# Performance work log

Measured on AMD Instinct MI355X. Metric: run time of the kernel, lower is better.

Reference implementation:

```python
import jax, jax.numpy as jnp
import numpy as np

DT = 0.001
TAU_SYN_INV = 200.0  # norse default 1/5e-3
TAU_MEM_INV = 100.0  # norse default 1/1e-2
V_TH = 0.4
ALPHA = 10.0  # SuperSpike surrogate slope


@jax.custom_vjp
def heaviside(x):
    # SuperSpike: heaviside forward, 1/(alpha*|x|+1)^2 surrogate backward
    return (x > 0).astype(x.dtype)

def _h_fwd(x):
    return heaviside(x), x

def _h_bwd(x, g):
    return (g / (ALPHA * jnp.abs(x) + 1.0) ** 2,)

heaviside.defvjp(_h_fwd, _h_bwd)


def conv(x, w, b, stride=1):
    y = jax.lax.conv_general_dilated(
        x, w, (stride, stride), 'VALID',
        dimension_numbers=('NCHW', 'OIHW', 'NCHW'))
    return y + b[None, :, None, None]


def maxpool2(x):
    return jax.lax.reduce_window(x, -jnp.inf, jax.lax.max, (1, 1, 2, 2), (1, 1, 2, 2), 'VALID')


def setup_inputs() -> dict:
    key = jax.random.key(0)
    ks = jax.random.split(key, 11)
    B, T, H, W = 32, 64, 64, 64
    num_classes = 10
    F = 96 * 12 * 12  # flattened encoder size = 13824
    HID = 128

    def u(k, shape, fan_in):
        bound = 1.0 / np.sqrt(fan_in)
        return jax.random.uniform(k, shape, jnp.float32, -bound, bound)

    return dict(
        x=jax.random.normal(ks[0], (B, T, 1, H, W), jnp.float32),
        w1=u(ks[1], (32, 1, 5, 5), 25), b1=u(ks[2], (32,), 25),
        w2=u(ks[3], (64, 32, 3, 3), 32 * 9), b2=u(ks[4], (64,), 32 * 9),
        w3=u(ks[5], (96, 64, 3, 3), 64 * 9), b3=u(ks[6], (96,), 64 * 9),
        w_in=jax.random.normal(ks[7], (HID, F), jnp.float32) / np.sqrt(F),
        w_rec=jax.random.normal(ks[8], (HID, HID), jnp.float32) / np.sqrt(HID),
        w_fc=u(ks[9], (num_classes, HID), HID),
        b_fc=u(ks[10], (num_classes,), HID),
    )


def reference(x, w1, b1, w2, b2, w3, b3, w_in, w_rec, w_fc, b_fc):
    B, T = x.shape[0], x.shape[1]
    HID = w_in.shape[0]
    C = w_fc.shape[0]

    # encoder vectorized over all B*T frames
    frames = x.reshape(B * T, x.shape[2], x.shape[3], x.shape[4])
    z = jax.nn.relu(conv(frames, w1, b1, stride=2))  # [BT,32,30,30]
    z = jax.nn.relu(conv(z, w2, b2))                 # [BT,64,28,28]
    z = maxpool2(z)                                  # [BT,64,14,14]
    z = jax.nn.relu(conv(z, w3, b3))                 # [BT,96,12,12]
    feats = z.reshape(B, T, -1)                      # [B,T,13824]

    # precompute feed-forward input currents for all timesteps
    ff = jnp.einsum('btf,hf->tbh', feats, w_in)      # [T,B,HID]

    def step(carry, ff_t):
        z_p, v, i, vr, ir = carry
        # LIF recurrent cell (norse lif_step, v_leak=0, v_reset=0)
        v_dec = v + DT * TAU_MEM_INV * (-v + i)
        i_dec = i - DT * TAU_SYN_INV * i
        z_n = heaviside(v_dec - V_TH)
        v_n = (1.0 - z_n) * v_dec
        i_n = i_dec + ff_t + z_p @ w_rec.T  # recurrent uses previous spikes
        # readout linear + LI cell (norse li_feed_forward_step)
        ro = z_n @ w_fc.T + b_fc
        vr_n = vr + DT * TAU_MEM_INV * (-vr + ir)
        ir_n = ir - DT * TAU_SYN_INV * ir + ro
        return (z_n, v_n, i_n, vr_n, ir_n), vr_n

    zeros_h = jnp.zeros((B, HID), x.dtype)
    zeros_c = jnp.zeros((B, C), x.dtype)
    carry0 = (zeros_h, zeros_h, zeros_h, zeros_c, zeros_c)
    _, voltages = jax.lax.scan(step, carry0, ff)     # [T,B,C]

    out = jnp.max(voltages, axis=0)                  # [B,C]
    return jax.nn.log_softmax(out, axis=1)
```

## Files before the change

### kernel.cpp

```cpp
#include <hip/hip_runtime.h>
#include <math.h>

typedef _Float16 half8 __attribute__((ext_vector_type(8)));
typedef _Float16 half4 __attribute__((ext_vector_type(4)));
typedef float f32x16 __attribute__((ext_vector_type(16)));

__global__ __launch_bounds__(256) void xprep_k(const float* __restrict__ x,
                                               _Float16* __restrict__ xh,
                                               _Float16* __restrict__ xl) {
  const int i = blockIdx.x * 256 + threadIdx.x;
  if (i >= 2097152) return;
  const float4 v = *(const float4*)(x + (size_t)i * 4);
  half4 h, l;
  const float vv[4] = {v.x, v.y, v.z, v.w};
#pragma unroll
  for (int e = 0; e < 4; ++e) {
    const _Float16 hh = (_Float16)vv[e];
    h[e] = hh;
    l[e] = (_Float16)((vv[e] - (float)hh) * 1024.0f);
  }
  *(half4*)(xh + (size_t)i * 4) = h;
  *(half4*)(xl + (size_t)i * 4) = l;
}

__global__ __launch_bounds__(256) void w1prep_k(const float* __restrict__ w1,
                                                _Float16* __restrict__ w1p) {
  const int i = blockIdx.x * 256 + threadIdx.x;
  if (i >= 1024) return;
  const int blk = i >> 8;
  const int s = blk >> 1, g = blk & 1;
  const int ch = (i >> 3) & 31, e = i & 7;
  const int k = s * 16 + g * 8 + e;
  float v = 0.f;
  if (k < 25) v = w1[ch * 25 + k];
  const _Float16 h = (_Float16)v;
  w1p[i] = h;
  w1p[1024 + i] = (_Float16)((v - (float)h) * 1024.0f);
}

__global__ __launch_bounds__(256) void w2prep_k(const float* __restrict__ w2,
                                                _Float16* __restrict__ w2p) {
  const int i = blockIdx.x * 256 + threadIdx.x;
  if (i >= 18432) return;
  const int tap = i >> 11;
  const int r = i & 2047;
  const int blk = r >> 8;
  const int nt = blk >> 2, s = (blk >> 1) & 1, g = blk & 1;
  const int n = (r >> 3) & 31, e = r & 7;
  const int och = nt * 32 + n;
  const int ic = s * 16 + g * 8 + e;
  const float v = w2[och * 288 + ic * 9 + tap];
  const _Float16 h = (_Float16)v;
  const _Float16 l = (_Float16)((v - (float)h) * 1024.0f);
  w2p[i] = h;
  w2p[18432 + i] = l;
}

__global__ __launch_bounds__(256) void w3prep_k(const float* __restrict__ w3,
                                                _Float16* __restrict__ w3p) {
  const int i = blockIdx.x * 256 + threadIdx.x;
  if (i >= 55296) return;
  const int icc = i / 27648;
  const int r1 = i - icc * 27648;
  const int tc = r1 / 6144;
  const int rem = r1 - tc * 6144;
  const int tl = rem / 3072;
  const int rem2 = rem - tl * 3072;
  const int nt = rem2 >> 10;
  const int s = (rem2 >> 9) & 1;
  const int g = (rem2 >> 8) & 1;
  const int n = (rem2 >> 3) & 31;
  const int e = rem2 & 7;
  const int tap = tc * 2 + tl;
  const int och = nt * 32 + n;
  const int ic = icc * 32 + s * 16 + g * 8 + e;
  const float v = w3[(size_t)och * 576 + ic * 9 + tap];
  const _Float16 h = (_Float16)v;
  const _Float16 l = (_Float16)((v - (float)h) * 1024.0f);
  w3p[i] = h;
  w3p[55296 + i] = l;
}

__global__ __launch_bounds__(256) void winprep_k(const float* __restrict__ w_in,
                                                 _Float16* __restrict__ winp) {
  const int i = blockIdx.x * 256 + threadIdx.x;
  if (i >= 1769472) return;
  const int ks = i >> 11;
  const int rem = i & 2047;
  const int nt = rem >> 9;
  const int g = (rem >> 8) & 1;
  const int n = (rem >> 3) & 31;
  const int e = rem & 7;
  const int h = nt * 32 + n;
  const int k = ks * 16 + g * 8 + e;
  const float v = w_in[(size_t)h * 13824 + k];
  const _Float16 hh = (_Float16)v;
  const _Float16 ll = (_Float16)((v - (float)hh) * 1024.0f);
  winp[i] = hh;
  winp[1769472 + i] = ll;
}

__global__ __launch_bounds__(448) void conv2f_mfma_k(
    const _Float16* __restrict__ xh, const _Float16* __restrict__ xl,
    const float* __restrict__ b1, const _Float16* __restrict__ w1p,
    const _Float16* __restrict__ w2p, const float* __restrict__ b2,
    _Float16* __restrict__ y2s) {
  __shared__ __align__(16) _Float16 S[24960];
  const int rp = blockIdx.x;
  const int img0 = blockIdx.y * 2;
  const int tid = threadIdx.x;

  const int w = tid >> 6;
  const int lane = tid & 63;
  const int l31 = lane & 31;
  const int g = lane >> 5;

  {
    const float b1c = b1[l31];
    const int gb = l31 >> 3, e0 = l31 & 7;
    int xoffs[16];
#pragma unroll
    for (int s = 0; s < 2; ++s)
#pragma unroll
      for (int e = 0; e < 8; ++e) {
        const int k = s * 16 + g * 8 + e;
        const int ky = k / 5, kx = k - (k / 5) * 5;
        xoffs[s * 8 + e] = (k < 25) ? (ky * 64 + kx) : -1;
      }
#pragma unroll 1
    for (int ph = 0; ph < 2; ++ph) {
      if (tid < 240) {
        const int plane = tid / 120;
        const int c8 = tid - plane * 120;
        const _Float16* src = (plane ? xl : xh) +
                              (size_t)(img0 + ph) * 4096 + rp * 512 + c8 * 8;
        *(float4*)&S[23040 + plane * 960 + c8 * 8] = *(const float4*)src;
      }
      __syncthreads();
      if (w < 6) {
        const int p = w * 32 + l31;
        const int pcl = (p < 180) ? p : 179;
        const int row = pcl / 30;
        const int col = pcl - row * 30;
        const int xb = (2 * row) * 64 + 2 * col;
        f32x16 acc_h = {}, acc_l = {};
#pragma unroll
        for (int s = 0; s < 2; ++s) {
          half8 ah, al;
#pragma unroll
          for (int e = 0; e < 8; ++e) {
            const int o = xoffs[s * 8 + e];
            _Float16 hv = (_Float16)0.f, lv = (_Float16)0.f;
            if (o >= 0) {
              hv = S[23040 + xb + o];
              lv = S[24000 + xb + o];
            }
            ah[e] = hv;
            al[e] = lv;
          }
          const _Float16* bp = w1p + ((s * 2 + g) * 32 + l31) * 8;
          half8 bh = *(const half8*)bp;
          half8 bl = *(const half8*)(bp + 1024);
          acc_h = __builtin_amdgcn_mfma_f32_32x32x16_f16(ah, bh, acc_h, 0, 0, 0);
          acc_l = __builtin_amdgcn_mfma_f32_32x32x16_f16(ah, bl, acc_l, 0, 0, 0);
          acc_l = __builtin_amdgcn_mfma_f32_32x32x16_f16(al, bh, acc_l, 0, 0, 0);
        }
#pragma unroll
        for (int r = 0; r < 16; ++r) {
          const int mrow = (r & 3) + 8 * (r >> 2) + 4 * g;
          const int pp = w * 32 + mrow;
          if (pp < 180) {
            const int cl = pp - (pp / 30) * 30;
            const int swz = (cl >> 1) & 3;
            const int addr = ph * 5760 + pp * 32 + ((gb ^ swz) << 3) + e0;
            const float val =
                fmaxf(acc_h[r] + acc_l[r] * 9.765625e-4f + b1c, 0.f);
            const _Float16 hh = (_Float16)val;
            S[addr] = hh;
            S[11520 + addr] = (_Float16)((val - (float)hh) * 1024.0f);
          }
        }
      }
      __syncthreads();
    }
  }

  const int m = w * 32 + l31;
  const int aimg = m / 112;
  const int apos = m - aimg * 112;
  const int ar = apos / 28;
  const int ax = apos - ar * 28;
  const int icg = g * 8;

  f32x16 acc00 = {}, acc01 = {}, acc10 = {}, acc11 = {};

  const _Float16* bb = w2p + g * 256 + l31 * 8;
  half8 pbh0, pbl0, pbh1, pbl1;
  half8 qbh0, qbl0, qbh1, qbl1;
  {
    pbh0 = *(const half8*)&bb[0];
    pbl0 = *(const half8*)&bb[18432];
    pbh1 = *(const half8*)&bb[1024];
    pbl1 = *(const half8*)&bb[18432 + 1024];
  }
#pragma unroll 1
  for (int i = 0; i < 18; i += 2) {
    {
      const int tap = (i + 1) >> 1, s = (i + 1) & 1;
      const _Float16* bt = bb + tap * 2048 + s * 512;
      qbh0 = *(const half8*)&bt[0];
      qbl0 = *(const half8*)&bt[18432];
      qbh1 = *(const half8*)&bt[1024];
      qbl1 = *(const half8*)&bt[18432 + 1024];
    }
    {
      const int tap = i >> 1, s = i & 1;
      const int ky = tap / 3, kx = tap - (tap / 3) * 3;
      const int acol = ax + kx;
      const int swzA = ((acol >> 1) & 3) << 3;
      const int abase = aimg * 5760 + ((ar + ky) * 30 + acol) * 32;
      const int icoA = (s * 16 + icg) ^ swzA;
      half8 ah = *(const half8*)&S[abase + icoA];
      half8 al = *(const half8*)&S[11520 + abase + icoA];
      acc00 = __builtin_amdgcn_mfma_f32_32x32x16_f16(ah, pbh0, acc00, 0, 0, 0);
      acc10 = __builtin_amdgcn_mfma_f32_32x32x16_f16(ah, pbl0, acc10, 0, 0, 0);
      acc10 = __builtin_amdgcn_mfma_f32_32x32x16_f16(al, pbh0, acc10, 0, 0, 0);
      acc01 = __builtin_amdgcn_mfma_f32_32x32x16_f16(ah, pbh1, acc01, 0, 0, 0);
      acc11 = __builtin_amdgcn_mfma_f32_32x32x16_f16(ah, pbl1, acc11, 0, 0, 0);
      acc11 = __builtin_amdgcn_mfma_f32_32x32x16_f16(al, pbh1, acc11, 0, 0, 0);
    }
    if (i + 2 < 18) {
      const int tap = (i + 2) >> 1, s = (i + 2) & 1;
      const _Float16* bt = bb + tap * 2048 + s * 512;
      pbh0 = *(const half8*)&bt[0];
      pbl0 = *(const half8*)&bt[18432];
      pbh1 = *(const half8*)&bt[1024];
      pbl1 = *(const half8*)&bt[18432 + 1024];
    }
    {
      const int ii = i + 1;
      const int tap = ii >> 1, s = ii & 1;
      const int ky = tap / 3, kx = tap - (tap / 3) * 3;
      const int acol = ax + kx;
      const int swzA = ((acol >> 1) & 3) << 3;
      const int abase = aimg * 5760 + ((ar + ky) * 30 + acol) * 32;
      const int icoA = (s * 16 + icg) ^ swzA;
      half8 ah = *(const half8*)&S[abase + icoA];
      half8 al = *(const half8*)&S[11520 + abase + icoA];
      acc00 = __builtin_amdgcn_mfma_f32_32x32x16_f16(ah, qbh0, acc00, 0, 0, 0);
      acc10 = __builtin_amdgcn_mfma_f32_32x32x16_f16(ah, qbl0, acc10, 0, 0, 0);
      acc10 = __builtin_amdgcn_mfma_f32_32x32x16_f16(al, qbh0, acc10, 0, 0, 0);
      acc01 = __builtin_amdgcn_mfma_f32_32x32x16_f16(ah, qbh1, acc01, 0, 0, 0);
      acc11 = __builtin_amdgcn_mfma_f32_32x32x16_f16(ah, qbl1, acc11, 0, 0, 0);
      acc11 = __builtin_amdgcn_mfma_f32_32x32x16_f16(al, qbh1, acc11, 0, 0, 0);
    }
  }

  float* sPool = (float*)S;
#pragma unroll 1
  for (int ph = 0; ph < 2; ++ph) {
    __syncthreads();
#pragma unroll
    for (int r = 0; r < 16; ++r) {
      const int mrow = (r & 3) + 8 * (r >> 2) + 4 * g;
      const int mo = w * 32 + mrow;
      const int srow = mo - ph * 112;
      if (srow >= 0 && srow < 112) {
        sPool[srow * 68 + l31] = acc00[r] + acc10[r] * 9.765625e-4f;
        sPool[srow * 68 + 32 + l31] = acc01[r] + acc11[r] * 9.765625e-4f;
      }
    }
    __syncthreads();
    if (tid < 224) {
      const int pr = tid / 112;
      const int r2 = tid - pr * 112;
      const int pc = r2 >> 3;
      const int blk = r2 & 7;
      const int m00 = pr * 56 + pc * 2;
      const float* s0 = &sPool[m00 * 68 + blk * 8];
      float rowv[4][8];
      *(float4*)&rowv[0][0] = *(const float4*)s0;
      *(float4*)&rowv[0][4] = *(const float4*)(s0 + 4);
      *(float4*)&rowv[1][0] = *(const float4*)(s0 + 68);
      *(float4*)&rowv[1][4] = *(const float4*)(s0 + 72);
      *(float4*)&rowv[2][0] = *(const float4*)(s0 + 28 * 68);
      *(float4*)&rowv[2][4] = *(const float4*)(s0 + 28 * 68 + 4);
      *(float4*)&rowv[3][0] = *(const float4*)(s0 + 29 * 68);
      *(float4*)&rowv[3][4] = *(const float4*)(s0 + 29 * 68 + 4);
      half8 hv, lv;
#pragma unroll
      for (int e = 0; e < 8; ++e) {
        const float mx = fmaxf(fmaxf(rowv[0][e], rowv[1][e]),
                               fmaxf(rowv[2][e], rowv[3][e]));
        const float val = fmaxf(mx + b2[blk * 8 + e], 0.f);
        const _Float16 hh = (_Float16)val;
        hv[e] = hh;
        lv[e] = (_Float16)((val - (float)hh) * 1024.0f);
      }
      const int posg = (rp * 2 + pr) * 14 + pc;
      const int icc = blk >> 2;
      const int slot = (blk & 3) ^ ((posg >> 1) & 3);
      _Float16* dh = y2s + (size_t)(img0 + ph) * 25088 + icc * 6272 +
                     posg * 32 + slot * 8;
      *(float4*)dh = *(float4*)&hv;
      *(float4*)(dh + 12544) = *(float4*)&lv;
    }
  }
}

__global__ __launch_bounds__(320) void conv3_mfma_k(
    const _Float16* __restrict__ y2s, const _Float16* __restrict__ w3p,
    const float* __restrict__ b3, _Float16* __restrict__ fh,
    _Float16* __restrict__ fl) {
  __shared__ __align__(16) _Float16 S[12544];
  const int img = blockIdx.x;
  const int tid = threadIdx.x;
  const int w = tid >> 6;
  const int lane = tid & 63;
  const int l31 = lane & 31;
  const int g = lane >> 5;
  const int m = w * 32 + l31;
  const int mc = (m < 144) ? m : 143;
  const int r = mc / 12, c = mc - (mc / 12) * 12;

  f32x16 acch[3] = {};
  f32x16 accl[3] = {};

  const _Float16* bb = w3p + g * 256 + l31 * 8;
#pragma unroll 1
  for (int icc = 0; icc < 2; ++icc) {
    __syncthreads();
    {
      const _Float16* src = y2s + (size_t)img * 25088 + icc * 6272;
      for (int c8 = tid; c8 < 784; c8 += 320) {
        *(float4*)&S[c8 * 8] = *(const float4*)&src[c8 * 8];
        *(float4*)&S[6272 + c8 * 8] = *(const float4*)&src[12544 + c8 * 8];
      }
    }
    __syncthreads();
#pragma unroll 1
    for (int tc = 0; tc < 5; ++tc) {
      const int ntaps = (tc == 4) ? 1 : 2;
#pragma unroll 1
      for (int tl = 0; tl < ntaps; ++tl) {
        const int tap = tc * 2 + tl;
        const int ky = tap / 3, kx = tap - (tap / 3) * 3;
        const int pix = (r + ky) * 14 + (c + kx);
        const int pswz = (pix >> 1) & 3;
        half8 ah[2], al[2];
#pragma unroll
        for (int s = 0; s < 2; ++s) {
          const int o = pix * 32 + ((s * 2 + g) ^ pswz) * 8;
          ah[s] = *(const half8*)&S[o];
          al[s] = *(const half8*)&S[6272 + o];
        }
        const _Float16* bt = bb + icc * 27648 + tc * 6144 + tl * 3072;
#pragma unroll
        for (int nt = 0; nt < 3; ++nt) {
#pragma unroll
          for (int s = 0; s < 2; ++s) {
            const _Float16* bp = bt + nt * 1024 + s * 512;
            half8 bh = *(const half8*)bp;
            half8 bl = *(const half8*)(bp + 55296);
            acch[nt] =
                __builtin_amdgcn_mfma_f32_32x32x16_f16(ah[s], bh, acch[nt], 0, 0, 0);
            accl[nt] =
                __builtin_amdgcn_mfma_f32_32x32x16_f16(ah[s], bl, accl[nt], 0, 0, 0);
            accl[nt] =
                __builtin_amdgcn_mfma_f32_32x32x16_f16(al[s], bh, accl[nt], 0, 0, 0);
          }
        }
      }
    }
  }
  float* sO = (float*)S;
#pragma unroll
  for (int nt = 0; nt < 3; ++nt) {
    __syncthreads();
#pragma unroll
    for (int rr = 0; rr < 16; ++rr) {
      const int row = (rr & 3) + 8 * (rr >> 2) + 4 * g;
      const int pos = w * 32 + row;
      if (pos < 144)
        sO[l31 * 145 + pos] = acch[nt][rr] + accl[nt][rr] * 9.765625e-4f;
    }
    __syncthreads();
    for (int idx8 = tid; idx8 < 576; idx8 += 320) {
      const int oc = idx8 / 18;
      const int pb = idx8 - oc * 18;
      const float bb2 = b3[nt * 32 + oc];
      half8 hv, lv;
#pragma unroll
      for (int e = 0; e < 8; ++e) {
        const float v = fmaxf(sO[oc * 145 + pb * 8 + e] + bb2, 0.f);
        const _Float16 hh = (_Float16)v;
        hv[e] = hh;
        lv[e] = (_Float16)((v - (float)hh) * 1024.0f);
      }
      const size_t ko = (size_t)img * 13824 + (nt * 32 + oc) * 144 + pb * 8;
      *(float4*)&fh[ko] = *(float4*)&hv;
      *(float4*)&fl[ko] = *(float4*)&lv;
    }
  }
}

__global__ __launch_bounds__(256) void ffgemm_k(
    const _Float16* __restrict__ fh, const _Float16* __restrict__ fl,
    const _Float16* __restrict__ winp, float* __restrict__ P, int frame0,
    int Cl) {
  __shared__ __align__(16) _Float16 S[24576];
  const int mb = blockIdx.x;
  const int kc = blockIdx.y;
  const int tid = threadIdx.x;
  const int w = tid >> 6;
  const int lane = tid & 63;
  const int l31 = lane & 31;
  const int g = lane >> 5;
  const int mt = w >> 1;
  const int nt0 = (w & 1) * 2;
  f32x16 acc_h[2] = {};
  f32x16 acc_l[2] = {};
  const int kbase = kc * 1728;
#pragma unroll 1
  for (int kt = 0; kt < 27; ++kt) {
    __syncthreads();
    for (int i = tid; i < 512; i += 256) {
      const int row = i >> 3, kb = i & 7;
      int rc = mb * 64 + row;
      if (rc >= Cl) rc = Cl - 1;
      const size_t so = (size_t)rc * 13824 + kbase + kt * 64 + kb * 8;
      const int d = row * 64 + ((kb ^ (row & 7)) * 8);
      *(float4*)&S[d] = *(const float4*)&fh[so];
      *(float4*)&S[4096 + d] = *(const float4*)&fl[so];
    }
    {
      const size_t bo = (size_t)(kc * 108 + kt * 4) * 2048;
      for (int i = tid; i < 1024; i += 256) {
        *(float4*)&S[8192 + i * 8] = *(const float4*)&winp[bo + i * 8];
        *(float4*)&S[16384 + i * 8] =
            *(const float4*)&winp[1769472 + bo + i * 8];
      }
    }
    __syncthreads();
#pragma unroll
    for (int ks = 0; ks < 4; ++ks) {
      const int kb = ks * 2 + g;
      const int ao = (mt * 32 + l31) * 64 + ((kb ^ (l31 & 7)) * 8);
      half8 ah = *(const half8*)&S[ao];
      half8 al = *(const half8*)&S[4096 + ao];
#pragma unroll
      for (int j = 0; j < 2; ++j) {
        const int nt = nt0 + j;
        const int b = 8192 + (((ks * 4 + nt) * 2 + g) * 32 + l31) * 8;
        half8 bh = *(const half8*)&S[b];
        half8 bl = *(const half8*)&S[8192 + b];
        acc_h[j] = __builtin_amdgcn_mfma_f32_32x32x16_f16(ah, bh, acc_h[j], 0, 0, 0);
        acc_l[j] = __builtin_amdgcn_mfma_f32_32x32x16_f16(ah, bl, acc_l[j], 0, 0, 0);
        acc_l[j] = __builtin_amdgcn_mfma_f32_32x32x16_f16(al, bh, acc_l[j], 0, 0, 0);
      }
    }
  }
  float* Pp = P + ((size_t)kc * 2048 + (size_t)frame0) * 128;
#pragma unroll
  for (int j = 0; j < 2; ++j) {
    const int h = (nt0 + j) * 32 + l31;
#pragma unroll
    for (int r = 0; r < 16; ++r) {
      const int row = (r & 3) + 8 * (r >> 2) + 4 * g;
      const int fr = mb * 64 + mt * 32 + row;
      if (fr < Cl)
        Pp[(size_t)fr * 128 + h] = acc_h[j][r] + acc_l[j][r] * 9.765625e-4f;
    }
  }
}

__global__ __launch_bounds__(256) void ffreduce_k(const float* __restrict__ P,
                                                  float* __restrict__ ffo) {
  const int i = blockIdx.x * 256 + threadIdx.x;
  float s = 0.f;
#pragma unroll
  for (int kcc = 0; kcc < 8; ++kcc) s += P[(size_t)kcc * 262144 + i];
  ffo[i] = s;
}

__global__ __launch_bounds__(64) void scan_k(
    const float* __restrict__ ff, const float* __restrict__ w_rec,
    const float* __restrict__ w_fc, const float* __restrict__ b_fc,
    float* __restrict__ out) {
#pragma clang fp contract(off)
  __shared__ float sWr[16384];
  const int b = blockIdx.x;
  const int t = threadIdx.x;
  for (int idx = t; idx < 16384; idx += 64) {
    int hh = idx >> 7, j = idx & 127;
    sWr[j * 128 + hh] = w_rec[idx];
  }
  float wf0[10], wf1[10], bf[10];
#pragma unroll
  for (int c = 0; c < 10; ++c) {
    wf0[c] = w_fc[c * 128 + t];
    wf1[c] = w_fc[c * 128 + 64 + t];
    bf[c] = b_fc[c];
  }
  __syncthreads();
  float v0 = 0.f, v1 = 0.f, i0 = 0.f, i1 = 0.f;
  float vr[10], ir[10], vmax[10];
#pragma unroll
  for (int c = 0; c < 10; ++c) {
    vr[c] = 0.f;
    ir[c] = 0.f;
    vmax[c] = -1e30f;
  }
  unsigned long long pm0 = 0ull, pm1 = 0ull;
  const float* ffb = ff + (size_t)b * 8192;
#pragma unroll 1
  for (int ts = 0; ts < 64; ++ts) {
    const float vd0 = v0 + 0.1f * (i0 - v0);
    const float vd1 = v1 + 0.1f * (i1 - v1);
    const float id0 = i0 - 0.2f * i0;
    const float id1 = i1 - 0.2f * i1;
    const bool z0 = (vd0 - 0.4f) > 0.f;
    const bool z1 = (vd1 - 0.4f) > 0.f;
    v0 = z0 ? 0.f : vd0;
    v1 = z1 ? 0.f : vd1;
    float rec0 = 0.f, rec1 = 0.f;
    unsigned long long mm = pm0;
    while (mm) {
      int j = __ffsll(mm) - 1;
      mm &= mm - 1;
      rec0 += sWr[j * 128 + t];
      rec1 += sWr[j * 128 + t + 64];
    }
    mm = pm1;
    while (mm) {
      int j = __ffsll(mm) - 1;
      mm &= mm - 1;
      rec0 += sWr[(j + 64) * 128 + t];
      rec1 += sWr[(j + 64) * 128 + t + 64];
    }
    i0 = (id0 + ffb[ts * 128 + t]) + rec0;
    i1 = (id1 + ffb[ts * 128 + 64 + t]) + rec1;
    pm0 = __ballot(z0);
    pm1 = __ballot(z1);
#pragma unroll
    for (int c = 0; c < 10; ++c) {
      float val = (z0 ? wf0[c] : 0.f) + (z1 ? wf1[c] : 0.f);
      val += __shfl_xor(val, 1);
      val += __shfl_xor(val, 2);
      val += __shfl_xor(val, 4);
      val += __shfl_xor(val, 8);
      val += __shfl_xor(val, 16);
      val += __shfl_xor(val, 32);
      const float ro = val + bf[c];
      vr[c] = vr[c] + 0.1f * (ir[c] - vr[c]);
      vmax[c] = fmaxf(vmax[c], vr[c]);
      ir[c] = (ir[c] - 0.2f * ir[c]) + ro;
    }
  }
  if (t == 0) {
    float M = vmax[0];
#pragma unroll
    for (int c = 1; c < 10; ++c) M = fmaxf(M, vmax[c]);
    float s = 0.f;
#pragma unroll
    for (int c = 0; c < 10; ++c) s += expf(vmax[c] - M);
    const float ls = logf(s);
#pragma unroll
    for (int c = 0; c < 10; ++c) out[b * 10 + c] = vmax[c] - M - ls;
  }
}

extern "C" void kernel_launch(void* const* d_in, const int* in_sizes, int n_in,
                              void* d_out, int out_size, void* d_ws,
                              size_t ws_size, hipStream_t stream) {
  (void)in_sizes;
  (void)n_in;
  (void)out_size;
  const float* x = (const float*)d_in[0];
  const float* w1 = (const float*)d_in[1];
  const float* b1 = (const float*)d_in[2];
  const float* w2 = (const float*)d_in[3];
  const float* b2 = (const float*)d_in[4];
  const float* w3 = (const float*)d_in[5];
  const float* b3 = (const float*)d_in[6];
  const float* w_in = (const float*)d_in[7];
  const float* w_rec = (const float*)d_in[8];
  const float* w_fc = (const float*)d_in[9];
  const float* b_fc = (const float*)d_in[10];
  float* out = (float*)d_out;
  char* ws = (char*)d_ws;

  const size_t OFF_W2P = 1048576ull + 8388608ull;
  const size_t OFF_W3P = OFF_W2P + 147456ull;
  const size_t OFF_WIN = OFF_W3P + 221184ull;
  const size_t OFF_W1P = OFF_WIN + 7077888ull;
  const size_t OFF_XH = OFF_W1P + 8192ull;
  const size_t OFF_XL = OFF_XH + 16777216ull;
  const size_t HDR = OFF_XL + 16777216ull;
  const size_t PERF = 50176ull + 55296ull;
  int C = 32;
  for (int c = 2048; c >= 32; c >>= 1) {
    if (HDR + (size_t)c * PERF <= ws_size) { C = c; break; }
  }
  float* ffbuf = (float*)ws;
  float* P = (float*)(ws + 1048576ull);
  _Float16* w2p = (_Float16*)(ws + OFF_W2P);
  _Float16* w3p = (_Float16*)(ws + OFF_W3P);
  _Float16* winp = (_Float16*)(ws + OFF_WIN);
  _Float16* w1p = (_Float16*)(ws + OFF_W1P);
  _Float16* xh = (_Float16*)(ws + OFF_XH);
  _Float16* xl = (_Float16*)(ws + OFF_XL);
  _Float16* y2s = (_Float16*)(ws + HDR);
  _Float16* fh = (_Float16*)(ws + HDR + (size_t)C * 50176ull);
  _Float16* fl = fh + (size_t)C * 13824;

  xprep_k<<<8192, 256, 0, stream>>>(x, xh, xl);
  w1prep_k<<<4, 256, 0, stream>>>(w1, w1p);
  w2prep_k<<<72, 256, 0, stream>>>(w2, w2p);
  w3prep_k<<<216, 256, 0, stream>>>(w3, w3p);
  winprep_k<<<6912, 256, 0, stream>>>(w_in, winp);

  const int nChunks = 2048 / C;
  const int mbN = (C + 63) / 64;
  for (int ch = 0; ch < nChunks; ++ch) {
    const int f0 = ch * C;
    conv2f_mfma_k<<<dim3(7, C / 2), 448, 0, stream>>>(
        xh + (size_t)f0 * 4096, xl + (size_t)f0 * 4096, b1, w1p, w2p, b2, y2s);
    conv3_mfma_k<<<C, 320, 0, stream>>>(y2s, w3p, b3, fh, fl);
    ffgemm_k<<<dim3(mbN, 8), 256, 0, stream>>>(fh, fl, winp, P, f0, C);
  }
  ffreduce_k<<<1024, 256, 0, stream>>>(P, ffbuf);
  scan_k<<<32, 64, 0, stream>>>(ffbuf, w_rec, w_fc, b_fc, out);
}
```

Baseline: 587.2 us.

## Stage conv2 weight taps through shared memory instead of per-wave global loads

The conv2 MFMA loop used to load B-operand weight fragments straight from global memory into registers, with software prefetch one step ahead. It now copies two taps at a time (high and low halves) cooperatively into an enlarged shared buffer, synchronises, and reads the fragments from LDS. This cuts redundant global/L2 traffic across the seven waves. In exchange it adds block barriers per tap pair, drops the register prefetch overlap, and raises LDS use, which may lower occupancy.

```diff
diff --git a/kernel.cpp b/kernel.cpp
--- a/kernel.cpp
+++ b/kernel.cpp
@@ -105,7 +105,7 @@
     const float* __restrict__ b1, const _Float16* __restrict__ w1p,
     const _Float16* __restrict__ w2p, const float* __restrict__ b2,
     _Float16* __restrict__ y2s) {
-  __shared__ __align__(16) _Float16 S[24960];
+  __shared__ __align__(16) _Float16 S[31232];
   const int rp = blockIdx.x;
   const int img0 = blockIdx.y * 2;
   const int tid = threadIdx.x;
@@ -194,65 +194,43 @@
 
   f32x16 acc00 = {}, acc01 = {}, acc10 = {}, acc11 = {};
 
-  const _Float16* bb = w2p + g * 256 + l31 * 8;
-  half8 pbh0, pbl0, pbh1, pbl1;
-  half8 qbh0, qbl0, qbh1, qbl1;
-  {
-    pbh0 = *(const half8*)&bb[0];
-    pbl0 = *(const half8*)&bb[18432];
-    pbh1 = *(const half8*)&bb[1024];
-    pbl1 = *(const half8*)&bb[18432 + 1024];
-  }
-#pragma unroll 1
-  for (int i = 0; i < 18; i += 2) {
-    {
-      const int tap = (i + 1) >> 1, s = (i + 1) & 1;
-      const _Float16* bt = bb + tap * 2048 + s * 512;
-      qbh0 = *(const half8*)&bt[0];
-      qbl0 = *(const half8*)&bt[18432];
-      qbh1 = *(const half8*)&bt[1024];
-      qbl1 = *(const half8*)&bt[18432 + 1024];
-    }
-    {
-      const int tap = i >> 1, s = i & 1;
-      const int ky = tap / 3, kx = tap - (tap / 3) * 3;
+#pragma unroll 1
+  for (int tc = 0; tc < 5; ++tc) {
+    __syncthreads();
+    const int tap0 = tc * 2;
+    const int ntaps = (tc == 4) ? 1 : 2;
+    for (int c = tid; c < ntaps * 256; c += 448) {
+      *(float4*)&S[23040 + c * 8] = *(const float4*)&w2p[tap0 * 2048 + c * 8];
+      *(float4*)&S[27136 + c * 8] =
+          *(const float4*)&w2p[18432 + tap0 * 2048 + c * 8];
+    }
+    __syncthreads();
+#pragma unroll 1
+    for (int tl = 0; tl < ntaps; ++tl) {
+      const int tap = tap0 + tl;
+      const int ky = tap / 3;
+      const int kx = tap - ky * 3;
       const int acol = ax + kx;
       const int swzA = ((acol >> 1) & 3) << 3;
       const int abase = aimg * 5760 + ((ar + ky) * 30 + acol) * 32;
-      const int icoA = (s * 16 + icg) ^ swzA;
-      half8 ah = *(const half8*)&S[abase + icoA];
-      half8 al = *(const half8*)&S[11520 + abase + icoA];
-      acc00 = __builtin_amdgcn_mfma_f32_32x32x16_f16(ah, pbh0, acc00, 0, 0, 0);
-      acc10 = __builtin_amdgcn_mfma_f32_32x32x16_f16(ah, pbl0, acc10, 0, 0, 0);
-      acc10 = __builtin_amdgcn_mfma_f32_32x32x16_f16(al, pbh0, acc10, 0, 0, 0);
-      acc01 = __builtin_amdgcn_mfma_f32_32x32x16_f16(ah, pbh1, acc01, 0, 0, 0);
-      acc11 = __builtin_amdgcn_mfma_f32_32x32x16_f16(ah, pbl1, acc11, 0, 0, 0);
-      acc11 = __builtin_amdgcn_mfma_f32_32x32x16_f16(al, pbh1, acc11, 0, 0, 0);
-    }
-    if (i + 2 < 18) {
-      const int tap = (i + 2) >> 1, s = (i + 2) & 1;
-      const _Float16* bt = bb + tap * 2048 + s * 512;
-      pbh0 = *(const half8*)&bt[0];
-      pbl0 = *(const half8*)&bt[18432];
-      pbh1 = *(const half8*)&bt[1024];
-      pbl1 = *(const half8*)&bt[18432 + 1024];
-    }
-    {
-      const int ii = i + 1;
-      const int tap = ii >> 1, s = ii & 1;
-      const int ky = tap / 3, kx = tap - (tap / 3) * 3;
-      const int acol = ax + kx;
-      const int swzA = ((acol >> 1) & 3) << 3;
-      const int abase = aimg * 5760 + ((ar + ky) * 30 + acol) * 32;
-      const int icoA = (s * 16 + icg) ^ swzA;
-      half8 ah = *(const half8*)&S[abase + icoA];
-      half8 al = *(const half8*)&S[11520 + abase + icoA];
-      acc00 = __builtin_amdgcn_mfma_f32_32x32x16_f16(ah, qbh0, acc00, 0, 0, 0);
-      acc10 = __builtin_amdgcn_mfma_f32_32x32x16_f16(ah, qbl0, acc10, 0, 0, 0);
-      acc10 = __builtin_amdgcn_mfma_f32_32x32x16_f16(al, qbh0, acc10, 0, 0, 0);
-      acc01 = __builtin_amdgcn_mfma_f32_32x32x16_f16(ah, qbh1, acc01, 0, 0, 0);
-      acc11 = __builtin_amdgcn_mfma_f32_32x32x16_f16(ah, qbl1, acc11, 0, 0, 0);
-      acc11 = __builtin_amdgcn_mfma_f32_32x32x16_f16(al, qbh1, acc11, 0, 0, 0);
+#pragma unroll
+      for (int s = 0; s < 2; ++s) {
+        const int icoA = (s * 16 + icg) ^ swzA;
+        const int bo0 = 23040 + (((tl * 2 + 0) * 2 + s) * 2 + g) * 256 + l31 * 8;
+        const int bo1 = 23040 + (((tl * 2 + 1) * 2 + s) * 2 + g) * 256 + l31 * 8;
+        half8 ah = *(const half8*)&S[abase + icoA];
+        half8 al = *(const half8*)&S[11520 + abase + icoA];
+        half8 bh0 = *(const half8*)&S[bo0];
+        half8 bl0 = *(const half8*)&S[bo0 + 4096];
+        half8 bh1 = *(const half8*)&S[bo1];
+        half8 bl1 = *(const half8*)&S[bo1 + 4096];
+        acc00 = __builtin_amdgcn_mfma_f32_32x32x16_f16(ah, bh0, acc00, 0, 0, 0);
+        acc10 = __builtin_amdgcn_mfma_f32_32x32x16_f16(ah, bl0, acc10, 0, 0, 0);
+        acc10 = __builtin_amdgcn_mfma_f32_32x32x16_f16(al, bh0, acc10, 0, 0, 0);
+        acc01 = __builtin_amdgcn_mfma_f32_32x32x16_f16(ah, bh1, acc01, 0, 0, 0);
+        acc11 = __builtin_amdgcn_mfma_f32_32x32x16_f16(ah, bl1, acc11, 0, 0, 0);
+        acc11 = __builtin_amdgcn_mfma_f32_32x32x16_f16(al, bh1, acc11, 0, 0, 0);
+      }
     }
   }
 
```

Result: no change. 592.7 us (+0.9%).
